# Optimization experiments

Hardware: AMD Instinct MI355X
Metric: run time of the kernel (lower is better)

Reference implementation:

```python
import jax, jax.numpy as jnp
import numpy as np

N_HEADS = 16


def build_bd3lm_mask(n, block_size, dtype):
    """BD3LM mask for concatenated [xt | x0] input of length 2n.
    0 = attend, finfo.min = masked. Shape (2n, 2n)."""
    idx = jnp.arange(2 * n)
    q_idx = idx[:, None]
    kv_idx = idx[None, :]
    x0_q = q_idx >= n
    x0_kv = kv_idx >= n
    block_q = jnp.where(x0_q, (q_idx - n) // block_size, q_idx // block_size)
    block_kv = jnp.where(x0_kv, (kv_idx - n) // block_size, kv_idx // block_size)
    block_diagonal = (block_q == block_kv) & (x0_q == x0_kv)
    offset_block_causal = (block_q > block_kv) & x0_kv & (~x0_q)
    block_causal = (block_q >= block_kv) & x0_kv & x0_q
    can_attend = block_diagonal | offset_block_causal | block_causal
    neg = jnp.finfo(dtype).min
    return jnp.where(can_attend, jnp.array(0, dtype), jnp.array(neg, dtype))


def setup_inputs() -> dict:
    key = jax.random.key(0)
    ks = jax.random.split(key, 5)
    B, T, D = 4, 2048, 1024  # T = 2*L, L = 1024
    s = 1.0 / np.sqrt(D)
    return {
        "x": jax.random.normal(ks[0], (B, T, D), jnp.float32),
        "Wq": jax.random.normal(ks[1], (D, D), jnp.float32) * s,
        "bq": jnp.zeros((D,), jnp.float32),
        "Wk": jax.random.normal(ks[2], (D, D), jnp.float32) * s,
        "bk": jnp.zeros((D,), jnp.float32),
        "Wv": jax.random.normal(ks[3], (D, D), jnp.float32) * s,
        "bv": jnp.zeros((D,), jnp.float32),
        "Wo": jax.random.normal(ks[4], (D, D), jnp.float32) * s,
        "bo": jnp.zeros((D,), jnp.float32),
        "block_size": 4,
    }


def reference(x, Wq, bq, Wk, bk, Wv, bv, Wo, bo, block_size):
    B, T, D = x.shape
    H = N_HEADS
    hd = D // H
    n = T // 2  # length of each copy in [xt | x0]
    mask = build_bd3lm_mask(n, block_size, x.dtype)  # (T, T)

    def split_heads(t):  # (B, T, D) -> (B, H, T, hd)
        return t.reshape(B, T, H, hd).transpose(0, 2, 1, 3)

    q = split_heads(x @ Wq + bq) * (hd ** -0.5)
    k = split_heads(x @ Wk + bk)
    v = split_heads(x @ Wv + bv)
    scores = jnp.einsum("bhqd,bhkd->bhqk", q, k) + mask[None, None]
    attn = jax.nn.softmax(scores, axis=-1)
    ctx = jnp.einsum("bhqk,bhkd->bhqd", attn, v)
    ctx = ctx.transpose(0, 2, 1, 3).reshape(B, T, D)
    return ctx @ Wo + bo
```

## Files before the change

kernel.cpp:

```cpp
#include <hip/hip_runtime.h>
#include <hip/hip_bf16.h>
#include <stdint.h>

typedef __hip_bfloat16 bf16;
typedef short v8s __attribute__((ext_vector_type(8)));
typedef float v4f __attribute__((ext_vector_type(4)));

#define TT   2048
#define DD   1024
#define HH   16
#define HDIM 64
#define NN   1024
#define MASKV (-1e9f)
#define QSCALE 0.18033688011112042f

#if __has_builtin(__builtin_amdgcn_exp2f)
#define EXP2F(x) __builtin_amdgcn_exp2f(x)
#else
#define EXP2F(x) exp2f(x)
#endif

__device__ __forceinline__ v4f mfma16x16x32(v8s a, v8s b, v4f c) {
    return __builtin_amdgcn_mfma_f32_16x16x32_bf16(a, b, c, 0, 0, 0);
}

template<bool SW>
__device__ __forceinline__ v4f MM(v8s a, v8s b, v4f c) {
    if constexpr (SW)
        return __builtin_amdgcn_mfma_f32_16x16x32_bf16(b, a, c, 0, 0, 0);
    else
        return __builtin_amdgcn_mfma_f32_16x16x32_bf16(a, b, c, 0, 0, 0);
}

#define GLDS16(lds, g)                                                          \
    __builtin_amdgcn_global_load_lds(                                           \
        (const __attribute__((address_space(1))) void*)(g),                     \
        (__attribute__((address_space(3))) void*)(lds), 16, 0, 0)

__device__ __forceinline__ bf16 f2b(float f) { return __float2bfloat16(f); }

__global__ __launch_bounds__(256) void cast_x(const float* __restrict__ x,
                                              bf16* __restrict__ xb)
{
    const size_t i = ((size_t)blockIdx.x * 256 + threadIdx.x) * 4;
    const float4 f = *(const float4*)(x + i);
    union { bf16 b[4]; uint64_t u; } cv;
    cv.b[0] = f2b(f.x); cv.b[1] = f2b(f.y); cv.b[2] = f2b(f.z); cv.b[3] = f2b(f.w);
    *(uint64_t*)(xb + i) = cv.u;
}

__global__ __launch_bounds__(256) void transpose_w(
    const float* __restrict__ w0, const float* __restrict__ w1,
    const float* __restrict__ w2, const float* __restrict__ w3,
    bf16* __restrict__ dst)
{
    __shared__ float tile[64][65];
    const float* src = (blockIdx.z == 0) ? w0 : (blockIdx.z == 1) ? w1
                      : (blockIdx.z == 2) ? w2 : w3;
    bf16* d = dst + (size_t)blockIdx.z * 1024 * 1024;
    const int r0 = blockIdx.y * 64, c0 = blockIdx.x * 64;
    const int tx = threadIdx.x, ty = threadIdx.y;
#pragma unroll
    for (int j = 0; j < 16; j++) {
        int r = ty + j * 4;
        tile[r][tx] = src[(size_t)(r0 + r) * 1024 + c0 + tx];
    }
    __syncthreads();
#pragma unroll
    for (int j = 0; j < 16; j++) {
        int r = ty + j * 4;
        d[(size_t)(c0 + r) * 1024 + r0 + tx] = f2b(tile[tx][r]);
    }
}

template<bool SW>
__device__ __forceinline__ void gemm_core_256x128(
    const bf16* __restrict__ A, const bf16* __restrict__ BT,
    const int m0, const int n0, const int K,
    bf16* __restrict__ As, bf16* __restrict__ Bs,
    v4f (&acc)[8][2])
{
    const int tid  = threadIdx.x;
    const int lane = tid & 63, wv = tid >> 6;
    const int quad = lane >> 4, c = lane & 15;
    const int wm = wv >> 2, wn = wv & 3;
    const int c7 = c & 7;
    const int NT = K >> 6;

    const int rloc = wv * 8 + (lane >> 3);
    const int gsw  = ((lane & 7) ^ ((lane >> 3) & 7)) << 3;
    const bf16* aSrc = A  + (size_t)(m0 + rloc) * K + gsw;
    const bf16* bSrc = BT + (size_t)(n0 + rloc) * K + gsw;

#pragma unroll
    for (int i = 0; i < 8; i++)
#pragma unroll
        for (int j = 0; j < 2; j++) acc[i][j] = (v4f){0.f, 0.f, 0.f, 0.f};

    auto stageA = [&](bf16* dst, int j, int kt) {
        const int mo = ((j & 1) << 7) | ((j >> 1) << 6);
        GLDS16(dst + (j * 64 + wv * 8) * 64, aSrc + (size_t)mo * K + kt * 64);
    };
    auto stageB = [&](bf16* dst, int j, int kt) {
        GLDS16(dst + (j * 64 + wv * 8) * 64, bSrc + (size_t)(j << 6) * K + kt * 64);
    };

    stageB(Bs, 0, 0); stageB(Bs, 1, 0);
    stageA(As, 0, 0); stageA(As, 1, 0); stageA(As, 2, 0); stageA(As, 3, 0);
    asm volatile("s_waitcnt vmcnt(2)" ::: "memory");
    asm volatile("s_barrier" ::: "memory");

#pragma unroll 1
    for (int kt = 0; kt < NT; ++kt) {
        bf16* Ac = As + (kt & 1) * 16384;
        bf16* Bc = Bs + (kt & 1) * 8192;
        bf16* An = As + ((kt & 1) ^ 1) * 16384;
        bf16* Bn = Bs + ((kt & 1) ^ 1) * 8192;
        const int ktn = (kt + 1 < NT) ? kt + 1 : kt;

        v8s bfr[2][2];
#pragma unroll
        for (int nt = 0; nt < 2; nt++)
#pragma unroll
            for (int kh = 0; kh < 2; kh++)
                bfr[nt][kh] = *(const v8s*)(Bc + (wn * 32 + nt * 16 + c) * 64
                                            + (((kh * 4 + quad) ^ c7) << 3));
        v8s af[4][2];
#pragma unroll
        for (int mt = 0; mt < 4; mt++)
#pragma unroll
            for (int kh = 0; kh < 2; kh++)
                af[mt][kh] = *(const v8s*)(Ac + (wm * 64 + mt * 16 + c) * 64
                                           + (((kh * 4 + quad) ^ c7) << 3));
        stageB(Bn, 0, ktn); stageB(Bn, 1, ktn); stageA(An, 0, ktn);
        asm volatile("s_barrier" ::: "memory");
        __builtin_amdgcn_s_setprio(1);
#pragma unroll
        for (int mt = 0; mt < 4; mt++)
#pragma unroll
            for (int nt = 0; nt < 2; nt++) {
                acc[mt][nt] = MM<SW>(af[mt][0], bfr[nt][0], acc[mt][nt]);
                acc[mt][nt] = MM<SW>(af[mt][1], bfr[nt][1], acc[mt][nt]);
            }
        __builtin_amdgcn_s_setprio(0);
        asm volatile("s_waitcnt vmcnt(3)" ::: "memory");
        asm volatile("s_barrier" ::: "memory");

#pragma unroll
        for (int mt = 0; mt < 4; mt++)
#pragma unroll
            for (int kh = 0; kh < 2; kh++)
                af[mt][kh] = *(const v8s*)(Ac + (128 + wm * 64 + mt * 16 + c) * 64
                                           + (((kh * 4 + quad) ^ c7) << 3));
        stageA(An, 1, ktn); stageA(An, 2, ktn); stageA(An, 3, ktn);
        asm volatile("s_barrier" ::: "memory");
        __builtin_amdgcn_s_setprio(1);
#pragma unroll
        for (int mt = 0; mt < 4; mt++)
#pragma unroll
            for (int nt = 0; nt < 2; nt++) {
                acc[4 + mt][nt] = MM<SW>(af[mt][0], bfr[nt][0], acc[4 + mt][nt]);
                acc[4 + mt][nt] = MM<SW>(af[mt][1], bfr[nt][1], acc[4 + mt][nt]);
            }
        __builtin_amdgcn_s_setprio(0);
        asm volatile("s_waitcnt vmcnt(2)" ::: "memory");
        asm volatile("s_barrier" ::: "memory");
    }
    asm volatile("s_waitcnt vmcnt(0)" ::: "memory");
}

__global__ __launch_bounds__(512, 2) void gemm_qkv(
    const bf16* __restrict__ A, const bf16* __restrict__ BT,
    const float* __restrict__ bq, const float* __restrict__ bk,
    const float* __restrict__ bv,
    bf16* __restrict__ qo, bf16* __restrict__ ko, bf16* __restrict__ vt)
{
    __shared__ __align__(16) bf16 As[2 * 256 * 64];
    __shared__ __align__(16) bf16 Bs[2 * 128 * 64];
    const int id  = blockIdx.x;
    const int fid = (id & 7) * 96 + (id >> 3);
    const int by  = fid / 24, bx = fid - by * 24;
    const int m0  = by * 256, n0 = bx * 128;
    const int type = n0 >> 10;

    v4f acc[8][2];
    if (type == 2) gemm_core_256x128<true >(A, BT, m0, n0, 1024, As, Bs, acc);
    else           gemm_core_256x128<false>(A, BT, m0, n0, 1024, As, Bs, acc);

    const int tid  = threadIdx.x;
    const int lane = tid & 63, wv = tid >> 6;
    const int quad = lane >> 4, c = lane & 15;
    const int wm = wv >> 2, wn = wv & 3;
    const int nbase = n0 & 1023;

    if (type < 2) {
        bf16* o = (type == 0) ? qo : ko;
        const float* bp = (type == 0) ? bq : bk;
        const float scale = (type == 0) ? QSCALE : 1.0f;
#pragma unroll
        for (int mt = 0; mt < 8; mt++)
#pragma unroll
            for (int nt = 0; nt < 2; nt++) {
                const int within = nbase + wn * 32 + nt * 16 + c;
                const int h = within >> 6, d = within & 63;
                const float bias = bp[within];
#pragma unroll
                for (int r = 0; r < 4; r++) {
                    const int row = m0 + wm * 128 + mt * 16 + quad * 4 + r;
                    const int b_ = row >> 11, t = row & 2047;
                    const int bh = b_ * HH + h;
                    o[((size_t)bh * TT + t) * HDIM + d] =
                        f2b((acc[mt][nt][r] + bias) * scale);
                }
            }
    } else {
        const int b_    = m0 >> 11;
        const int m0loc = m0 & 2047;
#pragma unroll
        for (int mt = 0; mt < 8; mt++) {
            const int t = m0loc + wm * 128 + mt * 16 + c;
#pragma unroll
            for (int nt = 0; nt < 2; nt++)
#pragma unroll
                for (int r = 0; r < 4; r++) {
                    const int within = nbase + wn * 32 + nt * 16 + quad * 4 + r;
                    const int h = within >> 6, d = within & 63;
                    const int bh = b_ * HH + h;
                    vt[((size_t)bh * HDIM + d) * TT + t] =
                        f2b(acc[mt][nt][r] + bv[within]);
                }
        }
    }
}

__global__ __launch_bounds__(512, 2) void gemm_out(
    const bf16* __restrict__ A, const bf16* __restrict__ BT,
    const float* __restrict__ bo, float* __restrict__ out)
{
    __shared__ __align__(16) bf16 As[2 * 256 * 64];
    __shared__ __align__(16) bf16 Bs[2 * 128 * 64];
    const int id  = blockIdx.x;
    const int fid = (id & 7) * 32 + (id >> 3);
    const int by  = fid >> 3, bx = fid & 7;
    const int m0  = by * 256, n0 = bx * 128;

    v4f acc[8][2];
    gemm_core_256x128<false>(A, BT, m0, n0, 1024, As, Bs, acc);

    const int tid  = threadIdx.x;
    const int lane = tid & 63, wv = tid >> 6;
    const int quad = lane >> 4, c = lane & 15;
    const int wm = wv >> 2, wn = wv & 3;

#pragma unroll
    for (int mt = 0; mt < 8; mt++)
#pragma unroll
        for (int nt = 0; nt < 2; nt++) {
            const int col = n0 + wn * 32 + nt * 16 + c;
            const float bias = bo[col];
#pragma unroll
            for (int r = 0; r < 4; r++) {
                const int row = m0 + wm * 128 + mt * 16 + quad * 4 + r;
                out[(size_t)row * 1024 + col] = acc[mt][nt][r] + bias;
            }
        }
}

__global__ __launch_bounds__(256, 4) void attn(
    const bf16* __restrict__ Q, const bf16* __restrict__ Kb,
    const bf16* __restrict__ VT, bf16* __restrict__ ctx,
    const int* __restrict__ bsp)
{
    __shared__ __align__(16) bf16 Kt[2][32 * 64];
    __shared__ __align__(16) bf16 Vt[2][64 * 32];
    __shared__ __align__(16) bf16 plds[4][2][16 * 32];

    const int bs = bsp[0];
    const float inv  = 1.0f / (float)bs;
    const float hinv = 0.5f * inv;
    const int tid = threadIdx.x, lane = tid & 63, wv = tid >> 6;
    const int quad = lane >> 4, c = lane & 15;
    const int bh = blockIdx.x & 63;
    const int j  = blockIdx.x >> 6;
    const int g_tbl[16] = {7,6,5,4, 0,1,2,3, 4,5,6,7, 3,2,1,0};
    const bool xt = j < 8;
    const int g  = g_tbl[j];
    const int q0g = (xt ? 0 : NN) + g * 128;

    const bf16* qp = Q  + (size_t)bh * TT * HDIM;
    const bf16* kp = Kb + (size_t)bh * TT * HDIM;
    const bf16* vp = VT + (size_t)bh * HDIM * TT;

    int d_lo = 0, nd = 0, nf = 0, b_lo = 0, nb = 0;
    if (xt) {
        d_lo = (bs * (q0g / bs)) & ~31;
        const int d_hi = min((bs * ((q0g + 127) / bs) + bs + 31) & ~31, NN);
        nd = (d_hi - d_lo) >> 5;
        const int f = bs * (q0g / bs);
        nf = f >> 5;
        b_lo = NN + (nf << 5);
        const int b_hi = NN + min((bs * ((q0g + 127) / bs) + 31) & ~31, NN);
        nb = (b_hi > b_lo) ? (b_hi - b_lo) >> 5 : 0;
    } else {
        const int q0l = q0g - NN;
        const int f = min(bs * (q0l / bs) + bs, NN);
        nf = f >> 5;
        b_lo = NN + (nf << 5);
        const int b_hi = NN + min((bs * ((q0l + 127) / bs) + bs + 31) & ~31, NN);
        nb = (b_hi > b_lo) ? (b_hi - b_lo) >> 5 : 0;
    }
    const int nc = nd + nf + nb;

    float bqv[2][4];
#pragma unroll
    for (int t = 0; t < 2; t++)
#pragma unroll
        for (int r = 0; r < 4; r++) {
            const int qrow = q0g + wv * 32 + t * 16 + quad * 4 + r;
            const int qloc = xt ? qrow : qrow - NN;
            bqv[t][r] = floorf(fmaf((float)qloc, inv, hinv));
        }

    v8s aq[2][2];
#pragma unroll
    for (int t = 0; t < 2; t++) {
        const int rowb = q0g + wv * 32 + t * 16;
        aq[t][0] = *(const v8s*)(qp + (size_t)(rowb + c) * HDIM + quad * 8);
        aq[t][1] = *(const v8s*)(qp + (size_t)(rowb + c) * HDIM + 32 + quad * 8);
    }

    v4f O[2][4];
#pragma unroll
    for (int t = 0; t < 2; t++)
#pragma unroll
        for (int dt = 0; dt < 4; dt++) O[t][dt] = (v4f){0.f, 0.f, 0.f, 0.f};
    float lr[2][4] = {{0.f,0.f,0.f,0.f},{0.f,0.f,0.f,0.f}};

    const int klrow = lane >> 3, ks8 = lane & 7;
    const bf16* kSrc0 = kp + (size_t)(wv * 8 + klrow) * HDIM + ((ks8 ^ klrow) << 3);
    const int vlrow = lane >> 2, vs8 = lane & 3;
    const bf16* vSrc0 = vp + (size_t)(wv * 16 + vlrow) * TT + ((vs8 ^ (vlrow & 3)) << 3);

    auto kb_of = [&](int i, int& kb, int& type) {
        if (i < nd)           { kb = d_lo + (i << 5);             type = 1; }
        else if (i < nd + nf) { kb = NN + ((i - nd) << 5);        type = 0; }
        else                  { kb = b_lo + ((i - nd - nf) << 5); type = xt ? 2 : 3; }
    };
    auto stage = [&](int i) {
        int kb, ty; kb_of(i, kb, ty);
        const int sel = i & 1;
        GLDS16(&Kt[sel][wv * 512], kSrc0 + (size_t)kb * HDIM);
        GLDS16(&Vt[sel][wv * 512], vSrc0 + kb);
    };

    stage(0);
    asm volatile("s_waitcnt vmcnt(0)" ::: "memory");
    asm volatile("s_barrier" ::: "memory");

    const int xk = c & 7, xv = c & 3;
    const int pquad = quad << 3;
#pragma unroll 1
    for (int i = 0; i < nc; i++) {
        int kb, type; kb_of(i, kb, type);
        const int sel = i & 1;
        const bf16* Kl = Kt[sel];
        const bf16* Vl = Vt[sel];

        const v8s k0a = *(const v8s*)(Kl + c * 64        + ((quad       ^ xk) << 3));
        const v8s k0b = *(const v8s*)(Kl + c * 64        + (((quad ^ 4) ^ xk) << 3));
        const v8s k1a = *(const v8s*)(Kl + (16 + c) * 64 + ((quad       ^ xk) << 3));
        const v8s k1b = *(const v8s*)(Kl + (16 + c) * 64 + (((quad ^ 4) ^ xk) << 3));
        v8s vf[4];
#pragma unroll
        for (int dt = 0; dt < 4; dt++)
            vf[dt] = *(const v8s*)(Vl + (dt * 16 + c) * 32 + ((quad ^ xv) << 3));

        if (i + 1 < nc) stage(i + 1);

        float bkA = 0.f, bkB = 0.f;
        if (type) {
            const int off = (type == 1) ? 0 : NN;
            bkA = floorf(fmaf((float)(kb + c - off),      inv, hinv));
            bkB = floorf(fmaf((float)(kb + 16 + c - off), inv, hinv));
        }

#pragma unroll
        for (int t = 0; t < 2; t++) {
            v4f Sa = (v4f){0.f, 0.f, 0.f, 0.f};
            v4f Sb = (v4f){0.f, 0.f, 0.f, 0.f};
            __builtin_amdgcn_s_setprio(1);
            Sa = mfma16x16x32(aq[t][0], k0a, Sa);
            Sa = mfma16x16x32(aq[t][1], k0b, Sa);
            Sb = mfma16x16x32(aq[t][0], k1a, Sb);
            Sb = mfma16x16x32(aq[t][1], k1b, Sb);
            __builtin_amdgcn_s_setprio(0);
            bf16* pw = &plds[wv][t][(quad * 4) * 32];
#pragma unroll
            for (int r = 0; r < 4; r++) {
                float sa = Sa[r], sb = Sb[r];
                if (type == 1) {
                    if (bkA != bqv[t][r]) sa = MASKV;
                    if (bkB != bqv[t][r]) sb = MASKV;
                } else if (type == 2) {
                    if (!(bkA < bqv[t][r])) sa = MASKV;
                    if (!(bkB < bqv[t][r])) sb = MASKV;
                } else if (type == 3) {
                    if (!(bkA <= bqv[t][r])) sa = MASKV;
                    if (!(bkB <= bqv[t][r])) sb = MASKV;
                }
                const float pa = EXP2F(sa);
                const float pb = EXP2F(sb);
                lr[t][r] += pa + pb;
                pw[r * 32 + (c ^ pquad)]        = f2b(pa);
                pw[r * 32 + ((c + 16) ^ pquad)] = f2b(pb);
            }
        }
        asm volatile("s_waitcnt lgkmcnt(0)" ::: "memory");
#pragma unroll
        for (int t = 0; t < 2; t++) {
            const v8s pf = *(const v8s*)(&plds[wv][t][c * 32 +
                                        ((quad ^ ((c >> 2) & 3)) << 3)]);
            __builtin_amdgcn_s_setprio(1);
#pragma unroll
            for (int dt = 0; dt < 4; dt++)
                O[t][dt] = mfma16x16x32(pf, vf[dt], O[t][dt]);
            __builtin_amdgcn_s_setprio(0);
        }

        asm volatile("s_waitcnt vmcnt(0)" ::: "memory");
        asm volatile("s_barrier" ::: "memory");
    }

    const int b_ = bh >> 4, h = bh & 15;
#pragma unroll
    for (int t = 0; t < 2; t++)
#pragma unroll
        for (int r = 0; r < 4; r++) {
            float s = lr[t][r];
#pragma unroll
            for (int off = 1; off < 16; off <<= 1) s += __shfl_xor(s, off);
            const float invl = 1.0f / fmaxf(s, 1e-30f);
            const int trow = q0g + wv * 32 + t * 16 + quad * 4 + r;
#pragma unroll
            for (int dt = 0; dt < 4; dt++)
                ctx[((size_t)(b_ * TT + trow)) * DD + h * 64 + dt * 16 + c] =
                    f2b(O[t][dt][r] * invl);
        }
}

extern "C" void kernel_launch(void* const* d_in, const int* in_sizes, int n_in,
                              void* d_out, int out_size, void* d_ws, size_t ws_size,
                              hipStream_t stream)
{
    const float* x  = (const float*)d_in[0];
    const float* Wq = (const float*)d_in[1];
    const float* bq = (const float*)d_in[2];
    const float* Wk = (const float*)d_in[3];
    const float* bk = (const float*)d_in[4];
    const float* Wv = (const float*)d_in[5];
    const float* bv = (const float*)d_in[6];
    const float* Wo = (const float*)d_in[7];
    const float* bo = (const float*)d_in[8];
    const int*  bsp = (const int*)d_in[9];
    float* out = (float*)d_out;

    bf16* ws    = (bf16*)d_ws;
    bf16* xb    = ws;
    bf16* wqkvT = xb + 8388608;
    bf16* woT   = wqkvT + 3 * 1024 * 1024;
    bf16* qbuf  = woT + 1024 * 1024;
    bf16* kbuf  = qbuf + 8388608;
    bf16* vt    = kbuf + 8388608;
    bf16* ctx   = xb;

    cast_x<<<8192, 256, 0, stream>>>(x, xb);
    transpose_w<<<dim3(16, 16, 4), dim3(64, 4), 0, stream>>>(Wq, Wk, Wv, Wo, wqkvT);
    gemm_qkv<<<768, 512, 0, stream>>>(xb, wqkvT, bq, bk, bv, qbuf, kbuf, vt);
    attn<<<1024, 256, 0, stream>>>(qbuf, kbuf, vt, ctx, bsp);
    gemm_out<<<256, 512, 0, stream>>>(ctx, woT, bo, out);
}
```

Before: 238.7 us.

## Rewrite GEMM core with BK=32 triple-buffered pipeline and smaller out tiles

Replaces the 256x128 BK=64 double-buffered GEMM core with a templated BK=32 core that uses a three-slot LDS ring, prefetching two k-tiles ahead with a single barrier per iteration. The warp layout changes to 4x2 with 4 N-subtiles per warp. LDS per block shrinks, and launch bounds are raised so more blocks can be resident per CU. gemm_out moves to 128x128 tiles with a 512-block grid to fill more CUs. The cost is more k-iterations, each with less MFMA work to hide global-load latency, plus changed register pressure under the tighter launch bounds.

```diff
diff --git a/kernel.cpp b/kernel.cpp
--- a/kernel.cpp
+++ b/kernel.cpp
@@ -73,124 +73,106 @@
     }
 }
 
-template<bool SW>
-__device__ __forceinline__ void gemm_core_256x128(
+template<int MT, bool SW>
+__device__ __forceinline__ void gemm_core_bk32(
     const bf16* __restrict__ A, const bf16* __restrict__ BT,
     const int m0, const int n0, const int K,
     bf16* __restrict__ As, bf16* __restrict__ Bs,
-    v4f (&acc)[8][2])
-{
+    v4f (&acc)[MT][4])
+{
+    constexpr int ACALLS = (MT * 64) / 128;
+    constexpr int CPT    = ACALLS + 1;
+    constexpr int ASLOT  = MT * 64 * 32;
+    constexpr int BSLOT  = 128 * 32;
+    const int NT = K >> 5;
+
     const int tid  = threadIdx.x;
     const int lane = tid & 63, wv = tid >> 6;
     const int quad = lane >> 4, c = lane & 15;
-    const int wm = wv >> 2, wn = wv & 3;
-    const int c7 = c & 7;
-    const int NT = K >> 6;
-
-    const int rloc = wv * 8 + (lane >> 3);
-    const int gsw  = ((lane & 7) ^ ((lane >> 3) & 7)) << 3;
-    const bf16* aSrc = A  + (size_t)(m0 + rloc) * K + gsw;
-    const bf16* bSrc = BT + (size_t)(n0 + rloc) * K + gsw;
-
-#pragma unroll
-    for (int i = 0; i < 8; i++)
-#pragma unroll
-        for (int j = 0; j < 2; j++) acc[i][j] = (v4f){0.f, 0.f, 0.f, 0.f};
-
-    auto stageA = [&](bf16* dst, int j, int kt) {
-        const int mo = ((j & 1) << 7) | ((j >> 1) << 6);
-        GLDS16(dst + (j * 64 + wv * 8) * 64, aSrc + (size_t)mo * K + kt * 64);
+    const int wm = wv >> 1, wn = wv & 1;
+    const int c3 = c & 3;
+
+    const int srow = wv * 16 + (lane >> 2);
+    const int sgr  = ((lane & 3) ^ ((lane >> 2) & 3)) << 3;
+    const bf16* aS = A  + (size_t)(m0 + srow) * K + sgr;
+    const bf16* bS = BT + (size_t)(n0 + srow) * K + sgr;
+
+    auto stage = [&](int t, int slot) {
+        const int k0 = t << 5;
+#pragma unroll
+        for (int j = 0; j < ACALLS; j++)
+            GLDS16(As + slot * ASLOT + j * 4096 + wv * 512,
+                   aS + (size_t)(j * 128) * K + k0);
+        GLDS16(Bs + slot * BSLOT + wv * 512, bS + k0);
     };
-    auto stageB = [&](bf16* dst, int j, int kt) {
-        GLDS16(dst + (j * 64 + wv * 8) * 64, bSrc + (size_t)(j << 6) * K + kt * 64);
-    };
-
-    stageB(Bs, 0, 0); stageB(Bs, 1, 0);
-    stageA(As, 0, 0); stageA(As, 1, 0); stageA(As, 2, 0); stageA(As, 3, 0);
-    asm volatile("s_waitcnt vmcnt(2)" ::: "memory");
+
+#pragma unroll
+    for (int i = 0; i < MT; i++)
+#pragma unroll
+        for (int j = 0; j < 4; j++) acc[i][j] = (v4f){0.f, 0.f, 0.f, 0.f};
+
+    stage(0, 0);
+    stage(1 < NT ? 1 : 0, 1);
+    if constexpr (CPT == 3) asm volatile("s_waitcnt vmcnt(3)" ::: "memory");
+    else                    asm volatile("s_waitcnt vmcnt(2)" ::: "memory");
     asm volatile("s_barrier" ::: "memory");
 
+    int slot = 0;
 #pragma unroll 1
-    for (int kt = 0; kt < NT; ++kt) {
-        bf16* Ac = As + (kt & 1) * 16384;
-        bf16* Bc = Bs + (kt & 1) * 8192;
-        bf16* An = As + ((kt & 1) ^ 1) * 16384;
-        bf16* Bn = Bs + ((kt & 1) ^ 1) * 8192;
-        const int ktn = (kt + 1 < NT) ? kt + 1 : kt;
-
-        v8s bfr[2][2];
-#pragma unroll
-        for (int nt = 0; nt < 2; nt++)
-#pragma unroll
-            for (int kh = 0; kh < 2; kh++)
-                bfr[nt][kh] = *(const v8s*)(Bc + (wn * 32 + nt * 16 + c) * 64
-                                            + (((kh * 4 + quad) ^ c7) << 3));
-        v8s af[4][2];
-#pragma unroll
-        for (int mt = 0; mt < 4; mt++)
-#pragma unroll
-            for (int kh = 0; kh < 2; kh++)
-                af[mt][kh] = *(const v8s*)(Ac + (wm * 64 + mt * 16 + c) * 64
-                                           + (((kh * 4 + quad) ^ c7) << 3));
-        stageB(Bn, 0, ktn); stageB(Bn, 1, ktn); stageA(An, 0, ktn);
+    for (int t = 0; t < NT; ++t) {
+        const int tn  = (t + 2 < NT) ? t + 2 : NT - 1;
+        const int sl2 = (slot >= 1) ? slot - 1 : 2;
+        stage(tn, sl2);
+
+        const bf16* Ac = As + slot * ASLOT;
+        const bf16* Bc = Bs + slot * BSLOT;
+        v8s af[MT], bfr[4];
+#pragma unroll
+        for (int mt = 0; mt < MT; mt++)
+            af[mt] = *(const v8s*)(Ac + (wm * (MT * 16) + mt * 16 + c) * 32
+                                   + ((quad ^ c3) << 3));
+#pragma unroll
+        for (int nt = 0; nt < 4; nt++)
+            bfr[nt] = *(const v8s*)(Bc + (wn * 64 + nt * 16 + c) * 32
+                                    + ((quad ^ c3) << 3));
+        __builtin_amdgcn_s_setprio(1);
+#pragma unroll
+        for (int mt = 0; mt < MT; mt++)
+#pragma unroll
+            for (int nt = 0; nt < 4; nt++)
+                acc[mt][nt] = MM<SW>(af[mt], bfr[nt], acc[mt][nt]);
+        __builtin_amdgcn_s_setprio(0);
+
+        if constexpr (CPT == 3) asm volatile("s_waitcnt vmcnt(3)" ::: "memory");
+        else                    asm volatile("s_waitcnt vmcnt(2)" ::: "memory");
         asm volatile("s_barrier" ::: "memory");
-        __builtin_amdgcn_s_setprio(1);
-#pragma unroll
-        for (int mt = 0; mt < 4; mt++)
-#pragma unroll
-            for (int nt = 0; nt < 2; nt++) {
-                acc[mt][nt] = MM<SW>(af[mt][0], bfr[nt][0], acc[mt][nt]);
-                acc[mt][nt] = MM<SW>(af[mt][1], bfr[nt][1], acc[mt][nt]);
-            }
-        __builtin_amdgcn_s_setprio(0);
-        asm volatile("s_waitcnt vmcnt(3)" ::: "memory");
-        asm volatile("s_barrier" ::: "memory");
-
-#pragma unroll
-        for (int mt = 0; mt < 4; mt++)
-#pragma unroll
-            for (int kh = 0; kh < 2; kh++)
-                af[mt][kh] = *(const v8s*)(Ac + (128 + wm * 64 + mt * 16 + c) * 64
-                                           + (((kh * 4 + quad) ^ c7) << 3));
-        stageA(An, 1, ktn); stageA(An, 2, ktn); stageA(An, 3, ktn);
-        asm volatile("s_barrier" ::: "memory");
-        __builtin_amdgcn_s_setprio(1);
-#pragma unroll
-        for (int mt = 0; mt < 4; mt++)
-#pragma unroll
-            for (int nt = 0; nt < 2; nt++) {
-                acc[4 + mt][nt] = MM<SW>(af[mt][0], bfr[nt][0], acc[4 + mt][nt]);
-                acc[4 + mt][nt] = MM<SW>(af[mt][1], bfr[nt][1], acc[4 + mt][nt]);
-            }
-        __builtin_amdgcn_s_setprio(0);
-        asm volatile("s_waitcnt vmcnt(2)" ::: "memory");
-        asm volatile("s_barrier" ::: "memory");
+        slot = (slot >= 2) ? 0 : slot + 1;
     }
     asm volatile("s_waitcnt vmcnt(0)" ::: "memory");
 }
 
-__global__ __launch_bounds__(512, 2) void gemm_qkv(
+__global__ __launch_bounds__(512, 4) void gemm_qkv(
     const bf16* __restrict__ A, const bf16* __restrict__ BT,
     const float* __restrict__ bq, const float* __restrict__ bk,
     const float* __restrict__ bv,
     bf16* __restrict__ qo, bf16* __restrict__ ko, bf16* __restrict__ vt)
 {
-    __shared__ __align__(16) bf16 As[2 * 256 * 64];
-    __shared__ __align__(16) bf16 Bs[2 * 128 * 64];
+    __shared__ __align__(16) bf16 As[3 * 256 * 32];
+    __shared__ __align__(16) bf16 Bs[3 * 128 * 32];
     const int id  = blockIdx.x;
     const int fid = (id & 7) * 96 + (id >> 3);
     const int by  = fid / 24, bx = fid - by * 24;
     const int m0  = by * 256, n0 = bx * 128;
     const int type = n0 >> 10;
 
-    v4f acc[8][2];
-    if (type == 2) gemm_core_256x128<true >(A, BT, m0, n0, 1024, As, Bs, acc);
-    else           gemm_core_256x128<false>(A, BT, m0, n0, 1024, As, Bs, acc);
+    v4f acc[4][4];
+    if (type == 2) gemm_core_bk32<4, true >(A, BT, m0, n0, 1024, As, Bs, acc);
+    else           gemm_core_bk32<4, false>(A, BT, m0, n0, 1024, As, Bs, acc);
 
     const int tid  = threadIdx.x;
     const int lane = tid & 63, wv = tid >> 6;
     const int quad = lane >> 4, c = lane & 15;
-    const int wm = wv >> 2, wn = wv & 3;
+    const int wm = wv >> 1, wn = wv & 1;
     const int nbase = n0 & 1023;
 
     if (type < 2) {
@@ -198,15 +180,15 @@
         const float* bp = (type == 0) ? bq : bk;
         const float scale = (type == 0) ? QSCALE : 1.0f;
 #pragma unroll
-        for (int mt = 0; mt < 8; mt++)
-#pragma unroll
-            for (int nt = 0; nt < 2; nt++) {
-                const int within = nbase + wn * 32 + nt * 16 + c;
+        for (int mt = 0; mt < 4; mt++)
+#pragma unroll
+            for (int nt = 0; nt < 4; nt++) {
+                const int within = nbase + wn * 64 + nt * 16 + c;
                 const int h = within >> 6, d = within & 63;
                 const float bias = bp[within];
 #pragma unroll
                 for (int r = 0; r < 4; r++) {
-                    const int row = m0 + wm * 128 + mt * 16 + quad * 4 + r;
+                    const int row = m0 + wm * 64 + mt * 16 + quad * 4 + r;
                     const int b_ = row >> 11, t = row & 2047;
                     const int bh = b_ * HH + h;
                     o[((size_t)bh * TT + t) * HDIM + d] =
@@ -217,13 +199,13 @@
         const int b_    = m0 >> 11;
         const int m0loc = m0 & 2047;
 #pragma unroll
-        for (int mt = 0; mt < 8; mt++) {
-            const int t = m0loc + wm * 128 + mt * 16 + c;
-#pragma unroll
-            for (int nt = 0; nt < 2; nt++)
+        for (int mt = 0; mt < 4; mt++) {
+            const int t = m0loc + wm * 64 + mt * 16 + c;
+#pragma unroll
+            for (int nt = 0; nt < 4; nt++)
 #pragma unroll
                 for (int r = 0; r < 4; r++) {
-                    const int within = nbase + wn * 32 + nt * 16 + quad * 4 + r;
+                    const int within = nbase + wn * 64 + nt * 16 + quad * 4 + r;
                     const int h = within >> 6, d = within & 63;
                     const int bh = b_ * HH + h;
                     vt[((size_t)bh * HDIM + d) * TT + t] =
@@ -233,34 +215,34 @@
     }
 }
 
-__global__ __launch_bounds__(512, 2) void gemm_out(
+__global__ __launch_bounds__(512, 4) void gemm_out(
     const bf16* __restrict__ A, const bf16* __restrict__ BT,
     const float* __restrict__ bo, float* __restrict__ out)
 {
-    __shared__ __align__(16) bf16 As[2 * 256 * 64];
-    __shared__ __align__(16) bf16 Bs[2 * 128 * 64];
+    __shared__ __align__(16) bf16 As[3 * 128 * 32];
+    __shared__ __align__(16) bf16 Bs[3 * 128 * 32];
     const int id  = blockIdx.x;
-    const int fid = (id & 7) * 32 + (id >> 3);
+    const int fid = (id & 7) * 64 + (id >> 3);
     const int by  = fid >> 3, bx = fid & 7;
-    const int m0  = by * 256, n0 = bx * 128;
-
-    v4f acc[8][2];
-    gemm_core_256x128<false>(A, BT, m0, n0, 1024, As, Bs, acc);
+    const int m0  = by * 128, n0 = bx * 128;
+
+    v4f acc[2][4];
+    gemm_core_bk32<2, false>(A, BT, m0, n0, 1024, As, Bs, acc);
 
     const int tid  = threadIdx.x;
     const int lane = tid & 63, wv = tid >> 6;
     const int quad = lane >> 4, c = lane & 15;
-    const int wm = wv >> 2, wn = wv & 3;
-
-#pragma unroll
-    for (int mt = 0; mt < 8; mt++)
-#pragma unroll
-        for (int nt = 0; nt < 2; nt++) {
-            const int col = n0 + wn * 32 + nt * 16 + c;
+    const int wm = wv >> 1, wn = wv & 1;
+
+#pragma unroll
+    for (int mt = 0; mt < 2; mt++)
+#pragma unroll
+        for (int nt = 0; nt < 4; nt++) {
+            const int col = n0 + wn * 64 + nt * 16 + c;
             const float bias = bo[col];
 #pragma unroll
             for (int r = 0; r < 4; r++) {
-                const int row = m0 + wm * 128 + mt * 16 + quad * 4 + r;
+                const int row = m0 + wm * 32 + mt * 16 + quad * 4 + r;
                 out[(size_t)row * 1024 + col] = acc[mt][nt][r] + bias;
             }
         }
@@ -477,5 +459,5 @@
     transpose_w<<<dim3(16, 16, 4), dim3(64, 4), 0, stream>>>(Wq, Wk, Wv, Wo, wqkvT);
     gemm_qkv<<<768, 512, 0, stream>>>(xb, wqkvT, bq, bk, bv, qbuf, kbuf, vt);
     attn<<<1024, 256, 0, stream>>>(qbuf, kbuf, vt, ctx, bsp);
-    gemm_out<<<256, 512, 0, stream>>>(ctx, woT, bo, out);
-}
+    gemm_out<<<512, 512, 0, stream>>>(ctx, woT, bo, out);
+}
```

After: 262.9 us. 1.1x slower.

## Stage K/V chunks in pairs to halve barriers in attention loop

Applied to the files above, without the earlier changes.

The attention main loop now prefetches two 32-key K/V chunks per stage into a doubled LDS buffer and computes both before one wait and barrier, instead of syncing after every chunk. This halves the number of s_waitcnt/s_barrier points and gives each prefetch a longer window to overlap with compute. In exchange, LDS use for K/V doubles, which may reduce occupancy at 4 blocks per CU. The prefetch is also issued before the current chunk's LDS reads, which changes when loads are in flight relative to those reads.

```diff
diff --git a/kernel.cpp b/kernel.cpp
--- a/kernel.cpp
+++ b/kernel.cpp
@@ -271,8 +271,8 @@
     const bf16* __restrict__ VT, bf16* __restrict__ ctx,
     const int* __restrict__ bsp)
 {
-    __shared__ __align__(16) bf16 Kt[2][32 * 64];
-    __shared__ __align__(16) bf16 Vt[2][64 * 32];
+    __shared__ __align__(16) bf16 Kt[2][2][32 * 64];
+    __shared__ __align__(16) bf16 Vt[2][2][64 * 32];
     __shared__ __align__(16) bf16 plds[4][2][16 * 32];
 
     const int bs = bsp[0];
@@ -346,25 +346,23 @@
         else if (i < nd + nf) { kb = NN + ((i - nd) << 5);        type = 0; }
         else                  { kb = b_lo + ((i - nd - nf) << 5); type = xt ? 2 : 3; }
     };
-    auto stage = [&](int i) {
-        int kb, ty; kb_of(i, kb, ty);
-        const int sel = i & 1;
-        GLDS16(&Kt[sel][wv * 512], kSrc0 + (size_t)kb * HDIM);
-        GLDS16(&Vt[sel][wv * 512], vSrc0 + kb);
+    auto stagePair = [&](int ip, int sel) {
+        const int c0 = ip * 2;
+        const int c1 = (c0 + 1 < nc) ? c0 + 1 : c0;
+        int kb, ty;
+        kb_of(c0, kb, ty);
+        GLDS16(&Kt[sel][0][wv * 512], kSrc0 + (size_t)kb * HDIM);
+        GLDS16(&Vt[sel][0][wv * 512], vSrc0 + kb);
+        kb_of(c1, kb, ty);
+        GLDS16(&Kt[sel][1][wv * 512], kSrc0 + (size_t)kb * HDIM);
+        GLDS16(&Vt[sel][1][wv * 512], vSrc0 + kb);
     };
-
-    stage(0);
-    asm volatile("s_waitcnt vmcnt(0)" ::: "memory");
-    asm volatile("s_barrier" ::: "memory");
 
     const int xk = c & 7, xv = c & 3;
     const int pquad = quad << 3;
-#pragma unroll 1
-    for (int i = 0; i < nc; i++) {
+
+    auto compute_chunk = [&](int i, const bf16* Kl, const bf16* Vl) {
         int kb, type; kb_of(i, kb, type);
-        const int sel = i & 1;
-        const bf16* Kl = Kt[sel];
-        const bf16* Vl = Vt[sel];
 
         const v8s k0a = *(const v8s*)(Kl + c * 64        + ((quad       ^ xk) << 3));
         const v8s k0b = *(const v8s*)(Kl + c * 64        + (((quad ^ 4) ^ xk) << 3));
@@ -374,8 +372,6 @@
 #pragma unroll
         for (int dt = 0; dt < 4; dt++)
             vf[dt] = *(const v8s*)(Vl + (dt * 16 + c) * 32 + ((quad ^ xv) << 3));
-
-        if (i + 1 < nc) stage(i + 1);
 
         float bkA = 0.f, bkB = 0.f;
         if (type) {
@@ -426,7 +422,20 @@
                 O[t][dt] = mfma16x16x32(pf, vf[dt], O[t][dt]);
             __builtin_amdgcn_s_setprio(0);
         }
-
+    };
+
+    const int npairs = (nc + 1) >> 1;
+    stagePair(0, 0);
+    asm volatile("s_waitcnt vmcnt(0)" ::: "memory");
+    asm volatile("s_barrier" ::: "memory");
+
+#pragma unroll 1
+    for (int ip = 0; ip < npairs; ip++) {
+        const int sel = ip & 1;
+        if (ip + 1 < npairs) stagePair(ip + 1, sel ^ 1);
+        compute_chunk(2 * ip, Kt[sel][0], Vt[sel][0]);
+        if (2 * ip + 1 < nc)
+            compute_chunk(2 * ip + 1, Kt[sel][1], Vt[sel][1]);
         asm volatile("s_waitcnt vmcnt(0)" ::: "memory");
         asm volatile("s_barrier" ::: "memory");
     }
```

After: 242.8 us. About the same (+1.7%).
